# Kernel optimization log

Measured on AMD Instinct MI355X. Metric: run time of the kernel, lower is better.

## Reference

```python
import jax, jax.numpy as jnp
import numpy as np

N, E = 10000, 30000
D_IN, E_DIM, H1, H2, C = 64, 16, 128, 64, 10


def setup_inputs() -> dict:
    key = jax.random.key(0)
    ks = jax.random.split(key, 12)
    x = jax.random.normal(ks[0], (N, D_IN), dtype=jnp.float32)
    edge_attr = jax.random.normal(ks[1], (E, E_DIM), dtype=jnp.float32)
    edge_index = jax.random.randint(ks[2], (2, E), 0, N, dtype=jnp.int64)
    # linear1: D_IN -> H1
    W1 = jax.random.normal(ks[3], (D_IN, H1), dtype=jnp.float32) / np.sqrt(D_IN)
    b1 = jnp.zeros((H1,), dtype=jnp.float32)
    # edge MLP 1: E_DIM -> H1*H2
    We1 = jax.random.normal(ks[4], (E_DIM, H1 * H2), dtype=jnp.float32) / np.sqrt(E_DIM)
    be1 = jnp.zeros((H1 * H2,), dtype=jnp.float32)
    root1 = jax.random.uniform(ks[5], (H1, H2), dtype=jnp.float32,
                               minval=-1.0 / np.sqrt(H1), maxval=1.0 / np.sqrt(H1))
    bias1 = jnp.zeros((H2,), dtype=jnp.float32)
    # edge MLP 2: E_DIM -> H2*C
    We2 = jax.random.normal(ks[6], (E_DIM, H2 * C), dtype=jnp.float32) / np.sqrt(E_DIM)
    be2 = jnp.zeros((H2 * C,), dtype=jnp.float32)
    root2 = jax.random.uniform(ks[7], (H2, C), dtype=jnp.float32,
                               minval=-1.0 / np.sqrt(H2), maxval=1.0 / np.sqrt(H2))
    bias2 = jnp.zeros((C,), dtype=jnp.float32)
    return {"x": x, "edge_attr": edge_attr, "edge_index": edge_index,
            "W1": W1, "b1": b1, "We1": We1, "be1": be1, "root1": root1, "bias1": bias1,
            "We2": We2, "be2": be2, "root2": root2, "bias2": bias2}


def _nnconv(h, src, dst, edge_attr, We, be, root, bias, c_in, c_out):
    # per-edge weight matrix from edge MLP: [E, c_in, c_out]
    W_e = (edge_attr @ We + be).reshape(-1, c_in, c_out)
    msg = jnp.einsum('ei,eio->eo', h[src], W_e)          # gather + batched matmul
    agg = jax.ops.segment_sum(msg, dst, num_segments=N)   # scatter-add to target nodes
    return agg + h @ root + bias


def reference(x, edge_attr, edge_index, W1, b1, We1, be1, root1, bias1,
              We2, be2, root2, bias2):
    src, dst = edge_index[0], edge_index[1]  # PyG: x_j = x[src], aggregate at dst
    h = jax.nn.relu(x @ W1 + b1)                               # [N, H1]
    h = jax.nn.relu(_nnconv(h, src, dst, edge_attr, We1, be1, root1, bias1, H1, H2))
    z = _nnconv(h, src, dst, edge_attr, We2, be2, root2, bias2, H2, C)
    return jax.nn.log_softmax(z, axis=1)
```

## Files before the change

### kernel.cpp

```cpp
#include <hip/hip_runtime.h>

#define N_NODES 10000
#define N_EDGES 30000
#define DIN     64
#define EDIM    16
#define H1      128
#define H2      64
#define C_OUT   10

typedef __bf16 bfrag __attribute__((ext_vector_type(8)));
typedef float  f32x4 __attribute__((ext_vector_type(4)));
typedef ushort ushort8 __attribute__((ext_vector_type(8)));

__device__ __forceinline__ ushort f2bf(float f) {
    union { float f; unsigned u; } x; x.f = f;
    unsigned r = x.u + 0x7fffu + ((x.u >> 16) & 1u);
    return (ushort)(r >> 16);
}
__device__ __forceinline__ float bf2f(ushort s) {
    union { unsigned u; float f; } x; x.u = ((unsigned)s) << 16;
    return x.f;
}

#define KA_B1   1250
#define KA_B2   (KA_B1 + 576)
#define KA_B3   (KA_B2 + 48)
__global__ __launch_bounds__(256) void kA_prep(
        const float* __restrict__ x, const float* __restrict__ W1,
        const float* __restrict__ b1,
        const float* __restrict__ We1, const float* __restrict__ root1,
        const float* __restrict__ be1,
        const float* __restrict__ We2, const float* __restrict__ be2,
        const float* __restrict__ root2,
        ushort* __restrict__ h_bf, ushort* __restrict__ B1t,
        ushort* __restrict__ B2t) {
    int t = threadIdx.x;
    int bx = blockIdx.x;
    if (bx < KA_B1) {
        __shared__ float w_lds[DIN * H1];
        __shared__ float b_lds[H1];
        __shared__ float x_lds[8][DIN];
        for (int idx = t; idx < DIN * H1 / 4; idx += 256)
            ((float4*)w_lds)[idx] = ((const float4*)W1)[idx];
        if (t < H1) b_lds[t] = b1[t];
        int n0 = bx * 8;
        if (t < 128) {
            int row = t >> 4, c4 = t & 15;
            int n = n0 + row;
            float4 v = make_float4(0.f, 0.f, 0.f, 0.f);
            if (n < N_NODES) v = ((const float4*)(x + (size_t)n * DIN))[c4];
            ((float4*)(x_lds[row]))[c4] = v;
        }
        __syncthreads();
        int nl = t >> 5;
        int o  = (t & 31) * 4;
        int n  = n0 + nl;
        float4 acc = *(const float4*)&b_lds[o];
        #pragma unroll 8
        for (int i = 0; i < DIN; ++i) {
            float xv = x_lds[nl][i];
            float4 w = *(const float4*)&w_lds[i * H1 + o];
            acc.x = fmaf(xv, w.x, acc.x);
            acc.y = fmaf(xv, w.y, acc.y);
            acc.z = fmaf(xv, w.z, acc.z);
            acc.w = fmaf(xv, w.w, acc.w);
        }
        if (n < N_NODES) {
            ushort4 s;
            s.x = f2bf(fmaxf(acc.x, 0.f));
            s.y = f2bf(fmaxf(acc.y, 0.f));
            s.z = f2bf(fmaxf(acc.z, 0.f));
            s.w = f2bf(fmaxf(acc.w, 0.f));
            *(ushort4*)&h_bf[(size_t)n * H1 + o] = s;
        }
    } else if (bx < KA_B2) {
        int idx = (bx - KA_B1) * 256 + t;
        int c = idx >> 7, i = idx & 127;
        float v;
        if (c < 1024) {
            int o = c >> 4, k = c & 15;
            v = We1[(size_t)k * (H1 * H2) + i * 64 + o];
        } else if (c < 1088) v = root1[i * 64 + (c - 1024)];
        else                 v = be1[i * 64 + (c - 1088)];
        B1t[idx] = f2bf(v);
    } else {
        int idx = (bx - KA_B2) * 256 + t;
        int c = idx >> 6, j = idx & 63;
        float v = 0.f;
        if (c < 160) {
            int cc = c >> 4, k = c & 15;
            v = We2[(size_t)k * 640 + j * 10 + cc];
        }
        else if (c < 170) v = be2[j * 10 + (c - 160)];
        else if (c < 180) v = root2[j * 10 + (c - 170)];
        B2t[idx] = f2bf(v);
    }
}

__global__ __launch_bounds__(256) void k3_mfma(
        const ushort* __restrict__ h_bf, const ushort* __restrict__ Bt,
        const float* __restrict__ bias1,
        ushort* __restrict__ G1t, float* __restrict__ hrb1, float* __restrict__ hb1,
        float* __restrict__ agg1, float* __restrict__ agg2) {
    int t = threadIdx.x;
    int wave = t >> 6, lane = t & 63;
    int quad = lane >> 4, lrow = lane & 15;
    int y = blockIdx.y;
    int mx = blockIdx.x;
    if (y == 17) {
        for (int i = mx * 256 + t; i < 160000; i += 79 * 256)
            ((float4*)agg1)[i] = make_float4(0.f, 0.f, 0.f, 0.f);
    } else if (y == 16) {
        for (int i = mx * 256 + t; i < 25000; i += 79 * 256)
            ((float4*)agg2)[i] = make_float4(0.f, 0.f, 0.f, 0.f);
    }
    int nbase = mx * 128 + wave * 32;
    int ar0 = nbase + lrow;       if (ar0 > N_NODES - 1) ar0 = N_NODES - 1;
    int ar1 = nbase + 16 + lrow;  if (ar1 > N_NODES - 1) ar1 = N_NODES - 1;
    const ushort* bbase = Bt + (size_t)y * 64 * 128;
    f32x4 acc0[4] = {}, acc1[4] = {};
    #pragma unroll
    for (int kc = 0; kc < 128; kc += 32) {
        bfrag a0 = *reinterpret_cast<const bfrag*>(h_bf + (size_t)ar0 * 128 + kc + quad * 8);
        bfrag a1 = *reinterpret_cast<const bfrag*>(h_bf + (size_t)ar1 * 128 + kc + quad * 8);
        #pragma unroll
        for (int ct = 0; ct < 4; ++ct) {
            bfrag b = *reinterpret_cast<const bfrag*>(
                bbase + (size_t)(ct * 16 + lrow) * 128 + kc + quad * 8);
            acc0[ct] = __builtin_amdgcn_mfma_f32_16x16x32_bf16(a0, b, acc0[ct], 0, 0, 0);
            acc1[ct] = __builtin_amdgcn_mfma_f32_16x16x32_bf16(a1, b, acc1[ct], 0, 0, 0);
        }
    }
    #pragma unroll
    for (int half = 0; half < 2; ++half) {
        int rbase = nbase + half * 16 + quad * 4;
        #pragma unroll
        for (int ct = 0; ct < 4; ++ct) {
            int col = ct * 16 + lrow;
            f32x4 a = half ? acc1[ct] : acc0[ct];
            #pragma unroll
            for (int r = 0; r < 4; ++r) {
                int n = rbase + r;
                if (n >= N_NODES) continue;
                float v = a[r];
                if (y < 16) {
                    G1t[(size_t)n * 1024 + y * 64 + col] = f2bf(v);
                } else if (y == 16) {
                    hrb1[(size_t)n * 64 + col] = v + bias1[col];
                } else {
                    hb1[(size_t)n * 64 + col] = v;
                }
            }
        }
    }
}

__global__ __launch_bounds__(256) void k4_edge1(
        const float* __restrict__ ea, const int* __restrict__ src_idx,
        const int* __restrict__ dst_idx, const ushort* __restrict__ G1t,
        const float* __restrict__ hb1, float* __restrict__ agg1) {
    int t = threadIdx.x;
    int e0 = blockIdx.x * 8 + (t >> 6) * 2;
    int o = t & 63;
    int s0 = src_idx[e0],     d0 = dst_idx[e0];
    int s1 = src_idx[e0 + 1], d1 = dst_idx[e0 + 1];
    const ushort* g0p = G1t + (size_t)s0 * 1024 + o * 16;
    const ushort* g1p = G1t + (size_t)s1 * 1024 + o * 16;
    ushort8 ga0 = *reinterpret_cast<const ushort8*>(g0p);
    ushort8 ga1 = *reinterpret_cast<const ushort8*>(g0p + 8);
    ushort8 gb0 = *reinterpret_cast<const ushort8*>(g1p);
    ushort8 gb1 = *reinterpret_cast<const ushort8*>(g1p + 8);
    float m0 = hb1[(size_t)s0 * 64 + o];
    float m1 = hb1[(size_t)s1 * 64 + o];
    const float* a0 = ea + (size_t)e0 * 16;
    const float* a1 = a0 + 16;
    #pragma unroll
    for (int k = 0; k < 8; ++k) {
        m0 = fmaf(a0[k], bf2f(ga0[k]), m0);
        m1 = fmaf(a1[k], bf2f(gb0[k]), m1);
    }
    #pragma unroll
    for (int k = 0; k < 8; ++k) {
        m0 = fmaf(a0[k + 8], bf2f(ga1[k]), m0);
        m1 = fmaf(a1[k + 8], bf2f(gb1[k]), m1);
    }
    atomicAdd(&agg1[(size_t)d0 * 64 + o], m0);
    atomicAdd(&agg1[(size_t)d1 * 64 + o], m1);
}

__global__ __launch_bounds__(256) void k56_mfma(
        const float* __restrict__ agg1, const float* __restrict__ hrb1,
        const ushort* __restrict__ B2t, const float* __restrict__ bias2,
        float* __restrict__ G2t, float* __restrict__ hb2, float* __restrict__ hr2) {
    int t = threadIdx.x;
    int wave = t >> 6, lane = t & 63;
    int quad = lane >> 4, lrow = lane & 15;
    int y = blockIdx.y;
    int n0 = blockIdx.x * 64 + wave * 16;
    int arow = n0 + lrow; if (arow > N_NODES - 1) arow = N_NODES - 1;
    f32x4 acc[4] = {};
    #pragma unroll
    for (int kc = 0; kc < 64; kc += 32) {
        size_t off = (size_t)arow * 64 + kc + quad * 8;
        f32x4 p0 = *(const f32x4*)(agg1 + off);
        f32x4 p1 = *(const f32x4*)(agg1 + off + 4);
        f32x4 q0 = *(const f32x4*)(hrb1 + off);
        f32x4 q1 = *(const f32x4*)(hrb1 + off + 4);
        bfrag a;
        #pragma unroll
        for (int j = 0; j < 4; ++j) {
            a[j]     = (__bf16)fmaxf(p0[j] + q0[j], 0.f);
            a[j + 4] = (__bf16)fmaxf(p1[j] + q1[j], 0.f);
        }
        #pragma unroll
        for (int ct = 0; ct < 4; ++ct) {
            bfrag b = *reinterpret_cast<const bfrag*>(
                B2t + (size_t)(y * 64 + ct * 16 + lrow) * 64 + kc + quad * 8);
            acc[ct] = __builtin_amdgcn_mfma_f32_16x16x32_bf16(a, b, acc[ct], 0, 0, 0);
        }
    }
    #pragma unroll
    for (int ct = 0; ct < 4; ++ct) {
        int cg = y * 64 + ct * 16 + lrow;
        #pragma unroll
        for (int r = 0; r < 4; ++r) {
            int n = n0 + quad * 4 + r;
            if (n >= N_NODES) continue;
            float v = acc[ct][r];
            if (cg < 160)      G2t[(size_t)n * 160 + cg] = v;
            else if (cg < 170) hb2[(size_t)n * 10 + (cg - 160)] = v;
            else if (cg < 180) hr2[(size_t)n * 10 + (cg - 170)] = v + bias2[cg - 170];
        }
    }
}

__global__ __launch_bounds__(256) void k7_edge2(
        const float* __restrict__ ea, const int* __restrict__ src_idx,
        const int* __restrict__ dst_idx, const float* __restrict__ G2t,
        const float* __restrict__ hb2, float* __restrict__ agg2) {
    int tid = blockIdx.x * 256 + threadIdx.x;
    if (tid >= N_EDGES * 10) return;
    int e = tid / 10, c = tid - e * 10;
    int s = src_idx[e], d = dst_idx[e];
    float m = hb2[(size_t)s * 10 + c];
    const float* g = G2t + (size_t)s * 160 + c * 16;
    const float* a = ea + (size_t)e * 16;
    f32x4 g0 = *(const f32x4*)g,       g1 = *(const f32x4*)(g + 4);
    f32x4 g2 = *(const f32x4*)(g + 8), g3 = *(const f32x4*)(g + 12);
    f32x4 a0 = *(const f32x4*)a,       a1 = *(const f32x4*)(a + 4);
    f32x4 a2 = *(const f32x4*)(a + 8), a3 = *(const f32x4*)(a + 12);
    #pragma unroll
    for (int k = 0; k < 4; ++k) {
        m = fmaf(a0[k], g0[k], m);
        m = fmaf(a1[k], g1[k], m);
        m = fmaf(a2[k], g2[k], m);
        m = fmaf(a3[k], g3[k], m);
    }
    atomicAdd(&agg2[(size_t)d * 10 + c], m);
}

__global__ void k8_logsoftmax(const float* __restrict__ agg2, const float* __restrict__ hr2,
                              float* __restrict__ out) {
    int n = blockIdx.x * blockDim.x + threadIdx.x;
    if (n >= N_NODES) return;
    float z[10]; float m = -1e30f;
    #pragma unroll
    for (int c = 0; c < 10; ++c) {
        z[c] = agg2[(size_t)n * 10 + c] + hr2[(size_t)n * 10 + c];
        m = fmaxf(m, z[c]);
    }
    float s = 0.f;
    #pragma unroll
    for (int c = 0; c < 10; ++c) s += expf(z[c] - m);
    float ls = logf(s);
    #pragma unroll
    for (int c = 0; c < 10; ++c) out[(size_t)n * 10 + c] = z[c] - m - ls;
}

extern "C" void kernel_launch(void* const* d_in, const int* in_sizes, int n_in,
                              void* d_out, int out_size, void* d_ws, size_t ws_size,
                              hipStream_t stream) {
    const float* x     = (const float*)d_in[0];
    const float* ea    = (const float*)d_in[1];
    const int*   eidx  = (const int*)d_in[2];
    const float* W1    = (const float*)d_in[3];
    const float* b1    = (const float*)d_in[4];
    const float* We1   = (const float*)d_in[5];
    const float* be1   = (const float*)d_in[6];
    const float* root1 = (const float*)d_in[7];
    const float* bias1 = (const float*)d_in[8];
    const float* We2   = (const float*)d_in[9];
    const float* be2   = (const float*)d_in[10];
    const float* root2 = (const float*)d_in[11];
    const float* bias2 = (const float*)d_in[12];
    float* out = (float*)d_out;

    float* ws = (float*)d_ws;
    ushort* h_bf = (ushort*)ws;
    ushort* B1t  = (ushort*)(ws + 640000);
    ushort* B2t  = (ushort*)(ws + 713728);
    ushort* G1t  = (ushort*)(ws + 719872);
    float* hrb1 = ws + 719872 + 5120000;
    float* hb1  = hrb1 + 640000;
    float* agg1 = hb1  + 640000;
    float* agg2 = agg1 + 640000;
    float* G2t  = agg2 + 100000;
    float* hb2  = G2t  + 1600000;
    float* hr2  = hb2  + 100000;

    kA_prep<<<KA_B3, 256, 0, stream>>>(x, W1, b1, We1, root1, be1, We2, be2, root2,
                                       h_bf, B1t, B2t);
    k3_mfma<<<dim3(79, 18), 256, 0, stream>>>(h_bf, B1t, bias1, G1t, hrb1, hb1,
                                              agg1, agg2);
    k4_edge1<<<3750, 256, 0, stream>>>(ea, eidx, eidx + N_EDGES, G1t, hb1, agg1);
    k56_mfma<<<dim3(157, 3), 256, 0, stream>>>(agg1, hrb1, B2t, bias2, G2t, hb2, hr2);
    k7_edge2<<<1172, 256, 0, stream>>>(ea, eidx, eidx + N_EDGES, G2t, hb2, agg2);
    k8_logsoftmax<<<40, 256, 0, stream>>>(agg2, hr2, out);
}
```

Measured before the change: 143.6 us.

## Fuse prep kernel into MFMA kernels, computing h and weight transposes per block

Removes the separate prep kernel. The first MFMA kernel now computes the x@W1 ReLU layer with MFMA into shared memory and builds its own slice of the transposed edge-MLP weights in LDS. The second MFMA kernel builds its own B2 tile in LDS. This saves one launch and the global round trip for h and the weight tables. In exchange, every block redundantly recomputes h for its rows (18 times over the y dimension) and redoes the strided weight transposes, and it uses more LDS per block.

```diff
diff --git a/kernel.cpp b/kernel.cpp
--- a/kernel.cpp
+++ b/kernel.cpp
@@ -22,91 +22,22 @@
     return x.f;
 }
 
-#define KA_B1   1250
-#define KA_B2   (KA_B1 + 576)
-#define KA_B3   (KA_B2 + 48)
-__global__ __launch_bounds__(256) void kA_prep(
+__global__ __launch_bounds__(256) void k3_mfma(
         const float* __restrict__ x, const float* __restrict__ W1,
         const float* __restrict__ b1,
         const float* __restrict__ We1, const float* __restrict__ root1,
-        const float* __restrict__ be1,
-        const float* __restrict__ We2, const float* __restrict__ be2,
-        const float* __restrict__ root2,
-        ushort* __restrict__ h_bf, ushort* __restrict__ B1t,
-        ushort* __restrict__ B2t) {
-    int t = threadIdx.x;
-    int bx = blockIdx.x;
-    if (bx < KA_B1) {
-        __shared__ float w_lds[DIN * H1];
-        __shared__ float b_lds[H1];
-        __shared__ float x_lds[8][DIN];
-        for (int idx = t; idx < DIN * H1 / 4; idx += 256)
-            ((float4*)w_lds)[idx] = ((const float4*)W1)[idx];
-        if (t < H1) b_lds[t] = b1[t];
-        int n0 = bx * 8;
-        if (t < 128) {
-            int row = t >> 4, c4 = t & 15;
-            int n = n0 + row;
-            float4 v = make_float4(0.f, 0.f, 0.f, 0.f);
-            if (n < N_NODES) v = ((const float4*)(x + (size_t)n * DIN))[c4];
-            ((float4*)(x_lds[row]))[c4] = v;
-        }
-        __syncthreads();
-        int nl = t >> 5;
-        int o  = (t & 31) * 4;
-        int n  = n0 + nl;
-        float4 acc = *(const float4*)&b_lds[o];
-        #pragma unroll 8
-        for (int i = 0; i < DIN; ++i) {
-            float xv = x_lds[nl][i];
-            float4 w = *(const float4*)&w_lds[i * H1 + o];
-            acc.x = fmaf(xv, w.x, acc.x);
-            acc.y = fmaf(xv, w.y, acc.y);
-            acc.z = fmaf(xv, w.z, acc.z);
-            acc.w = fmaf(xv, w.w, acc.w);
-        }
-        if (n < N_NODES) {
-            ushort4 s;
-            s.x = f2bf(fmaxf(acc.x, 0.f));
-            s.y = f2bf(fmaxf(acc.y, 0.f));
-            s.z = f2bf(fmaxf(acc.z, 0.f));
-            s.w = f2bf(fmaxf(acc.w, 0.f));
-            *(ushort4*)&h_bf[(size_t)n * H1 + o] = s;
-        }
-    } else if (bx < KA_B2) {
-        int idx = (bx - KA_B1) * 256 + t;
-        int c = idx >> 7, i = idx & 127;
-        float v;
-        if (c < 1024) {
-            int o = c >> 4, k = c & 15;
-            v = We1[(size_t)k * (H1 * H2) + i * 64 + o];
-        } else if (c < 1088) v = root1[i * 64 + (c - 1024)];
-        else                 v = be1[i * 64 + (c - 1088)];
-        B1t[idx] = f2bf(v);
-    } else {
-        int idx = (bx - KA_B2) * 256 + t;
-        int c = idx >> 6, j = idx & 63;
-        float v = 0.f;
-        if (c < 160) {
-            int cc = c >> 4, k = c & 15;
-            v = We2[(size_t)k * 640 + j * 10 + cc];
-        }
-        else if (c < 170) v = be2[j * 10 + (c - 160)];
-        else if (c < 180) v = root2[j * 10 + (c - 170)];
-        B2t[idx] = f2bf(v);
-    }
-}
-
-__global__ __launch_bounds__(256) void k3_mfma(
-        const ushort* __restrict__ h_bf, const ushort* __restrict__ Bt,
-        const float* __restrict__ bias1,
+        const float* __restrict__ be1, const float* __restrict__ bias1,
         ushort* __restrict__ G1t, float* __restrict__ hrb1, float* __restrict__ hb1,
         float* __restrict__ agg1, float* __restrict__ agg2) {
+    __shared__ ushort W1L[128 * 72];
+    __shared__ ushort B1L[64 * 136];
+    __shared__ ushort hL[128 * 136];
+    __shared__ float  b1L[H1];
     int t = threadIdx.x;
     int wave = t >> 6, lane = t & 63;
     int quad = lane >> 4, lrow = lane & 15;
-    int y = blockIdx.y;
-    int mx = blockIdx.x;
+    int y = blockIdx.y, mx = blockIdx.x;
+
     if (y == 17) {
         for (int i = mx * 256 + t; i < 160000; i += 79 * 256)
             ((float4*)agg1)[i] = make_float4(0.f, 0.f, 0.f, 0.f);
@@ -114,23 +45,80 @@
         for (int i = mx * 256 + t; i < 25000; i += 79 * 256)
             ((float4*)agg2)[i] = make_float4(0.f, 0.f, 0.f, 0.f);
     }
-    int nbase = mx * 128 + wave * 32;
-    int ar0 = nbase + lrow;       if (ar0 > N_NODES - 1) ar0 = N_NODES - 1;
-    int ar1 = nbase + 16 + lrow;  if (ar1 > N_NODES - 1) ar1 = N_NODES - 1;
-    const ushort* bbase = Bt + (size_t)y * 64 * 128;
+
+    for (int idx = t; idx < DIN * H1; idx += 256) {
+        int i = idx >> 7, o = idx & 127;
+        W1L[o * 72 + i] = f2bf(W1[idx]);
+    }
+    for (int idx = t; idx < 64 * 128; idx += 256) {
+        int c = idx >> 7, i = idx & 127;
+        float v;
+        if (y < 16) {
+            int cg = y * 64 + c;
+            v = We1[(size_t)(cg & 15) * (H1 * H2) + i * 64 + (cg >> 4)];
+        } else if (y == 16) v = root1[i * 64 + c];
+        else                v = be1[i * 64 + c];
+        B1L[c * 136 + i] = f2bf(v);
+    }
+    if (t < H1) b1L[t] = b1[t];
+    __syncthreads();
+
+    int nb = mx * 128;
+    int r0 = nb + wave * 32 + lrow;      if (r0 > N_NODES - 1) r0 = N_NODES - 1;
+    int r1 = r0 + 16;                    if (r1 > N_NODES - 1) r1 = N_NODES - 1;
+    bfrag xa[2][2];
+    #pragma unroll
+    for (int half = 0; half < 2; ++half) {
+        int rr = half ? r1 : r0;
+        #pragma unroll
+        for (int kk = 0; kk < 2; ++kk) {
+            f32x4 p = *(const f32x4*)(x + (size_t)rr * DIN + kk * 32 + quad * 8);
+            f32x4 q = *(const f32x4*)(x + (size_t)rr * DIN + kk * 32 + quad * 8 + 4);
+            bfrag a;
+            #pragma unroll
+            for (int j = 0; j < 4; ++j) { a[j] = (__bf16)p[j]; a[j + 4] = (__bf16)q[j]; }
+            xa[half][kk] = a;
+        }
+    }
+    #pragma unroll
+    for (int ct2 = 0; ct2 < 8; ++ct2) {
+        f32x4 ah0 = {}, ah1 = {};
+        #pragma unroll
+        for (int kk = 0; kk < 2; ++kk) {
+            bfrag b = *reinterpret_cast<const bfrag*>(
+                &W1L[(ct2 * 16 + lrow) * 72 + kk * 32 + quad * 8]);
+            ah0 = __builtin_amdgcn_mfma_f32_16x16x32_bf16(xa[0][kk], b, ah0, 0, 0, 0);
+            ah1 = __builtin_amdgcn_mfma_f32_16x16x32_bf16(xa[1][kk], b, ah1, 0, 0, 0);
+        }
+        int col = ct2 * 16 + lrow;
+        float bv = b1L[col];
+        #pragma unroll
+        for (int half = 0; half < 2; ++half) {
+            #pragma unroll
+            for (int r = 0; r < 4; ++r) {
+                int rl = wave * 32 + half * 16 + quad * 4 + r;
+                float v = (half ? ah1[r] : ah0[r]) + bv;
+                hL[rl * 136 + col] = f2bf(fmaxf(v, 0.f));
+            }
+        }
+    }
+
     f32x4 acc0[4] = {}, acc1[4] = {};
     #pragma unroll
     for (int kc = 0; kc < 128; kc += 32) {
-        bfrag a0 = *reinterpret_cast<const bfrag*>(h_bf + (size_t)ar0 * 128 + kc + quad * 8);
-        bfrag a1 = *reinterpret_cast<const bfrag*>(h_bf + (size_t)ar1 * 128 + kc + quad * 8);
+        bfrag a0 = *reinterpret_cast<const bfrag*>(
+            &hL[(wave * 32 + lrow) * 136 + kc + quad * 8]);
+        bfrag a1 = *reinterpret_cast<const bfrag*>(
+            &hL[(wave * 32 + 16 + lrow) * 136 + kc + quad * 8]);
         #pragma unroll
         for (int ct = 0; ct < 4; ++ct) {
             bfrag b = *reinterpret_cast<const bfrag*>(
-                bbase + (size_t)(ct * 16 + lrow) * 128 + kc + quad * 8);
+                &B1L[(ct * 16 + lrow) * 136 + kc + quad * 8]);
             acc0[ct] = __builtin_amdgcn_mfma_f32_16x16x32_bf16(a0, b, acc0[ct], 0, 0, 0);
             acc1[ct] = __builtin_amdgcn_mfma_f32_16x16x32_bf16(a1, b, acc1[ct], 0, 0, 0);
         }
     }
+    int nbase = nb + wave * 32;
     #pragma unroll
     for (int half = 0; half < 2; ++half) {
         int rbase = nbase + half * 16 + quad * 4;
@@ -190,12 +178,24 @@
 
 __global__ __launch_bounds__(256) void k56_mfma(
         const float* __restrict__ agg1, const float* __restrict__ hrb1,
-        const ushort* __restrict__ B2t, const float* __restrict__ bias2,
+        const float* __restrict__ We2, const float* __restrict__ be2,
+        const float* __restrict__ root2, const float* __restrict__ bias2,
         float* __restrict__ G2t, float* __restrict__ hb2, float* __restrict__ hr2) {
+    __shared__ ushort B2L[64 * 72];
     int t = threadIdx.x;
     int wave = t >> 6, lane = t & 63;
     int quad = lane >> 4, lrow = lane & 15;
     int y = blockIdx.y;
+    for (int idx = t; idx < 64 * 64; idx += 256) {
+        int c = idx >> 6, j = idx & 63;
+        int cg = y * 64 + c;
+        float v = 0.f;
+        if (cg < 160)      v = We2[(size_t)(cg & 15) * 640 + j * 10 + (cg >> 4)];
+        else if (cg < 170) v = be2[j * 10 + (cg - 160)];
+        else if (cg < 180) v = root2[j * 10 + (cg - 170)];
+        B2L[c * 72 + j] = f2bf(v);
+    }
+    __syncthreads();
     int n0 = blockIdx.x * 64 + wave * 16;
     int arow = n0 + lrow; if (arow > N_NODES - 1) arow = N_NODES - 1;
     f32x4 acc[4] = {};
@@ -215,7 +215,7 @@
         #pragma unroll
         for (int ct = 0; ct < 4; ++ct) {
             bfrag b = *reinterpret_cast<const bfrag*>(
-                B2t + (size_t)(y * 64 + ct * 16 + lrow) * 64 + kc + quad * 8);
+                &B2L[(ct * 16 + lrow) * 72 + kc + quad * 8]);
             acc[ct] = __builtin_amdgcn_mfma_f32_16x16x32_bf16(a, b, acc[ct], 0, 0, 0);
         }
     }
@@ -296,11 +296,8 @@
     float* out = (float*)d_out;
 
     float* ws = (float*)d_ws;
-    ushort* h_bf = (ushort*)ws;
-    ushort* B1t  = (ushort*)(ws + 640000);
-    ushort* B2t  = (ushort*)(ws + 713728);
-    ushort* G1t  = (ushort*)(ws + 719872);
-    float* hrb1 = ws + 719872 + 5120000;
+    ushort* G1t  = (ushort*)ws;
+    float* hrb1 = ws + 5120000;
     float* hb1  = hrb1 + 640000;
     float* agg1 = hb1  + 640000;
     float* agg2 = agg1 + 640000;
@@ -308,12 +305,11 @@
     float* hb2  = G2t  + 1600000;
     float* hr2  = hb2  + 100000;
 
-    kA_prep<<<KA_B3, 256, 0, stream>>>(x, W1, b1, We1, root1, be1, We2, be2, root2,
-                                       h_bf, B1t, B2t);
-    k3_mfma<<<dim3(79, 18), 256, 0, stream>>>(h_bf, B1t, bias1, G1t, hrb1, hb1,
-                                              agg1, agg2);
+    k3_mfma<<<dim3(79, 18), 256, 0, stream>>>(x, W1, b1, We1, root1, be1, bias1,
+                                              G1t, hrb1, hb1, agg1, agg2);
     k4_edge1<<<3750, 256, 0, stream>>>(ea, eidx, eidx + N_EDGES, G1t, hb1, agg1);
-    k56_mfma<<<dim3(157, 3), 256, 0, stream>>>(agg1, hrb1, B2t, bias2, G2t, hb2, hr2);
+    k56_mfma<<<dim3(157, 3), 256, 0, stream>>>(agg1, hrb1, We2, be2, root2, bias2,
+                                               G2t, hb2, hr2);
     k7_edge2<<<1172, 256, 0, stream>>>(ea, eidx, eidx + N_EDGES, G2t, hb2, agg2);
     k8_logsoftmax<<<40, 256, 0, stream>>>(agg2, hr2, out);
 }
```

New measurement: 174.7 us. +21.6%, slower.
